# Performance work log

Measured on AMD Instinct MI355X. Metric: run time of the kernel, lower is better.

## Reference

```python
import jax, jax.numpy as jnp
import numpy as np

T, B = 128, 256
WD, TD, RD, M = 300, 64, 64, 512
G = 5 * M  # 5 gates: i, f_down, f_left, o, u


def setup_inputs() -> dict:
    key = jax.random.key(0)
    ks = jax.random.split(key, 13)
    s = 0.05  # weight scale for numerical sanity
    return {
        "word": jax.random.normal(ks[0], (T, B, WD), jnp.float32),
        "tag": jax.random.normal(ks[1], (T, B, TD), jnp.float32),
        "rel": jax.random.normal(ks[2], (T, B, RD), jnp.float32),
        "k": jax.random.normal(ks[3], (T, B, M), jnp.float32),
        "q": jax.random.normal(ks[4], (T, B, M), jnp.float32),
        "h0": jnp.zeros((B, M), jnp.float32),
        "c0": jnp.zeros((B, M), jnp.float32),
        "Ww": jax.random.normal(ks[5], (WD, G), jnp.float32) * s,
        "Wt": jax.random.normal(ks[6], (TD, G), jnp.float32) * s,
        "Wr": jax.random.normal(ks[7], (RD, G), jnp.float32) * s,
        "Wk": jax.random.normal(ks[8], (M, G), jnp.float32) * s,
        "Wh": jax.random.normal(ks[9], (M, G), jnp.float32) * s,
        "b": jax.random.normal(ks[10], (G,), jnp.float32) * s,
    }


def reference(word, tag, rel, k, q, h0, c0, Ww, Wt, Wr, Wk, Wh, b):
    mem = h0.shape[-1]
    # Fuse all non-recurrent projections for all 5 gates into one pass:
    # [T,B,5M] preactivations from word/tag/rel/k (the per-child inputs).
    xp = (jnp.einsum('tbd,dg->tbg', word, Ww)
          + jnp.einsum('tbd,dg->tbg', tag, Wt)
          + jnp.einsum('tbd,dg->tbg', rel, Wr)
          + jnp.einsum('tbd,dg->tbg', k, Wk)
          + b)

    def step(carry, inp):
        h, c = carry
        xpt, qt = inp  # [B,5M], [B,M]
        g = xpt + h @ Wh
        gi, gfd, gfl, go, gu = (g[..., 0*mem:1*mem], g[..., 1*mem:2*mem],
                                g[..., 2*mem:3*mem], g[..., 3*mem:4*mem],
                                g[..., 4*mem:5*mem])
        i_ = jax.nn.sigmoid(gi)
        f_down = jax.nn.sigmoid(gfd)
        f_left = jax.nn.sigmoid(gfl)
        o_ = jax.nn.sigmoid(go)
        u_ = jnp.tanh(gu)
        c_new = i_ * u_ + f_down * qt + f_left * c
        h_new = o_ * jnp.tanh(c_new)
        return (h_new, c_new), None

    (h, c), _ = jax.lax.scan(step, (h0, c0), (xp, q))
    # node_forward returns (k, q) = (h, c) after consuming all children
    return jnp.concatenate([h, c], axis=-1)  # [B, 2*M]
```

## Files before the change

kernel.cpp:

```cpp
#include <hip/hip_runtime.h>
#include <hip/hip_bf16.h>

#define TT   128
#define BB   256
#define MM   512
#define GG   2560
#define K1P  960

typedef __attribute__((ext_vector_type(8))) short bf16x8;
typedef __attribute__((ext_vector_type(4))) short bf16x4;
typedef __attribute__((ext_vector_type(4))) float f32x4;

__device__ __forceinline__ float bf2f(unsigned short u){
  union { unsigned u; float f; } v; v.u = ((unsigned)u) << 16; return v.f;
}
__device__ __forceinline__ unsigned short f2bf(float f){
  union { float f; unsigned u; } v; v.f = f;
  unsigned r = v.u + 0x7fffu + ((v.u >> 16) & 1u);
  return (unsigned short)(r >> 16);
}
__device__ __forceinline__ float sigmoidf_(float x){ return 1.f/(1.f + __expf(-x)); }
__device__ __forceinline__ float tanhf_(float x){
  x = fminf(15.f, fmaxf(-15.f, x));
  float e = __expf(2.f*x);
  return (e - 1.f)/(e + 1.f);
}

__device__ __forceinline__ void store_coh4(void* p, unsigned v){
  asm volatile("global_store_dword %0, %1, off sc0 sc1" :: "v"(p), "v"(v) : "memory");
}
__device__ __forceinline__ unsigned load_coh_u32(const unsigned* p){
  unsigned r;
  asm volatile("global_load_dword %0, %1, off sc0 sc1" : "=v"(r) : "v"(p) : "memory");
  asm volatile("s_waitcnt vmcnt(0)" ::: "memory");
  return r;
}
__device__ __forceinline__ bf16x8 load_h16(const void* p){
  bf16x8 r;
  asm volatile("global_load_dwordx4 %0, %1, off sc0 sc1" : "=v"(r) : "v"(p) : "memory");
  return r;
}
__device__ __forceinline__ void store_h32(void* p, unsigned v){
  asm volatile("global_store_dword %0, %1, off sc0 sc1" :: "v"(p), "v"(v) : "memory");
}

__device__ __forceinline__ void gll16(const unsigned short* g, unsigned short* l){
  __builtin_amdgcn_global_load_lds(
      (const __attribute__((address_space(1))) void*)(g),
      (__attribute__((address_space(3))) void*)(l),
      16, 0, 0);
}


__global__ __launch_bounds__(256) void stage_a(const float* __restrict__ word,
                                               const float* __restrict__ tag,
                                               const float* __restrict__ rel,
                                               const float* __restrict__ kin,
                                               unsigned short* __restrict__ A){
  long id = (long)blockIdx.x * 256 + threadIdx.x;
  int row = (int)(id / 120);
  int c8  = (int)(id % 120) * 8;
  bf16x8 o;
  #pragma unroll
  for (int j = 0; j < 8; ++j){
    int col = c8 + j; float v;
    if      (col < 300) v = word[(long)row*300 + col];
    else if (col < 364) v = tag [(long)row*64  + col-300];
    else if (col < 428) v = rel [(long)row*64  + col-364];
    else if (col < 940) v = kin [(long)row*512 + col-428];
    else v = 0.f;
    o[j] = (short)f2bf(v);
  }
  *reinterpret_cast<bf16x8*>(A + (long)row*K1P + c8) = o;
}

__global__ __launch_bounds__(256) void stage_wt(const float* __restrict__ Ww,
                                                const float* __restrict__ Wt,
                                                const float* __restrict__ Wr,
                                                const float* __restrict__ Wk,
                                                unsigned short* __restrict__ WT){
  long id = (long)blockIdx.x * 256 + threadIdx.x;
  int kk = (int)(id % K1P);
  int n  = (int)(id / K1P);
  float v;
  if      (kk < 300) v = Ww[(long)kk*GG + n];
  else if (kk < 364) v = Wt[(long)(kk-300)*GG + n];
  else if (kk < 428) v = Wr[(long)(kk-364)*GG + n];
  else if (kk < 940) v = Wk[(long)(kk-428)*GG + n];
  else v = 0.f;
  WT[(long)n*K1P + kk] = f2bf(v);
}

__global__ __launch_bounds__(256) void stage_wht(const float* __restrict__ Wh,
                                                 unsigned short* __restrict__ WhT){
  long id = (long)blockIdx.x * 256 + threadIdx.x;
  int kk = (int)(id % MM);
  int n  = (int)(id / MM);
  WhT[(long)n*MM + kk] = f2bf(Wh[(long)kk*GG + n]);
}

__global__ __launch_bounds__(256) void init_h(const float* __restrict__ h0,
                                              unsigned short* __restrict__ hb){
  int id = blockIdx.x * 256 + threadIdx.x;
  hb[id] = f2bf(h0[id]);
}

__global__ __launch_bounds__(256) void gemm_xp(const unsigned short* __restrict__ A,
                                               const unsigned short* __restrict__ WT,
                                               const float* __restrict__ bias,
                                               unsigned short* __restrict__ XP){
  __shared__ unsigned short As[128*64];
  __shared__ unsigned short Bs[128*64];
  const int tid  = threadIdx.x;
  const int wave = tid >> 6, lane = tid & 63;
  const int wr   = wave >> 1, wc = wave & 1;
  const int lrow = lane & 15, lhi = lane >> 4;

  const int swz = (blockIdx.x & 7) * (5120 / 8) + (blockIdx.x >> 3);
  const long row0 = (long)(swz & 255) * 128;
  const long col0 = (long)(swz >> 8) * 128;

  const int srow = wave*8 + (lane >> 3);
  const int scol = (((lane & 7) ^ (lane >> 3)) * 8);
  const unsigned short* gaB = A  + (row0 + srow)*K1P + scol;
  const unsigned short* gbB = WT + (col0 + srow)*K1P + scol;

  f32x4 acc[4][4] = {};
  for (int ks = 0; ks < 15; ++ks){
    const int k0 = ks * 64;
    __syncthreads();
    #pragma unroll
    for (int s = 0; s < 4; ++s){
      gll16(gaB + (long)s*32*K1P + k0, As + (s*32 + wave*8)*64);
      gll16(gbB + (long)s*32*K1P + k0, Bs + (s*32 + wave*8)*64);
    }
    __syncthreads();
    bf16x8 af[2][4], bfr[2][4];
    const int sx = (lrow & 7) * 8;
    #pragma unroll
    for (int kk = 0; kk < 2; ++kk){
      #pragma unroll
      for (int mi = 0; mi < 4; ++mi)
        af[kk][mi] = *reinterpret_cast<const bf16x8*>(
            As + (wr*64 + mi*16 + lrow)*64 + ((kk*32 + lhi*8) ^ sx));
      #pragma unroll
      for (int ni = 0; ni < 4; ++ni)
        bfr[kk][ni] = *reinterpret_cast<const bf16x8*>(
            Bs + (wc*64 + ni*16 + lrow)*64 + ((kk*32 + lhi*8) ^ sx));
    }
    #pragma unroll
    for (int kk = 0; kk < 2; ++kk)
      #pragma unroll
      for (int mi = 0; mi < 4; ++mi)
        #pragma unroll
        for (int ni = 0; ni < 4; ++ni)
          acc[mi][ni] = __builtin_amdgcn_mfma_f32_16x16x32_bf16(af[kk][mi], bfr[kk][ni], acc[mi][ni], 0, 0, 0);
  }
  const int t     = (int)(row0 >> 8);
  const int brow0 = (int)(row0 & 255);
  #pragma unroll
  for (int ni = 0; ni < 4; ++ni){
    const int col = (int)col0 + wc*64 + ni*16 + lrow;
    const float bv = bias[col];
    #pragma unroll
    for (int mi = 0; mi < 4; ++mi){
      const int b4 = brow0 + wr*64 + mi*16 + lhi*4;
      bf16x4 pk;
      #pragma unroll
      for (int j = 0; j < 4; ++j) pk[j] = (short)f2bf(acc[mi][ni][j] + bv);
      *reinterpret_cast<bf16x4*>(XP + ((long)t*GG + col)*BB + b4) = pk;
    }
  }
}

__global__ __launch_bounds__(256, 1) void lstm_fused(const unsigned short* __restrict__ XP,
                                                     const float* __restrict__ q,
                                                     const unsigned short* __restrict__ WhT,
                                                     const float* __restrict__ c0,
                                                     unsigned short* __restrict__ hb0,
                                                     unsigned short* __restrict__ hb1,
                                                     float* __restrict__ out,
                                                     unsigned* __restrict__ cnts){
  __shared__ float Part[4][5][2][16][20];
  const int tid  = threadIdx.x;
  const int w    = tid >> 6, lane = tid & 63;
  const int lrow = lane & 15, lhi = lane >> 4;
  const int bt = blockIdx.x >> 5, mc = blockIdx.x & 31;
  const int b0 = bt * 32, m0 = mc * 16;
  unsigned* cnt = cnts + bt * 64;

  bf16x8 Breg[5][4];
  #pragma unroll
  for (int g = 0; g < 5; ++g)
    #pragma unroll
    for (int kf = 0; kf < 4; ++kf)
      Breg[g][kf] = *reinterpret_cast<const bf16x8*>(
          WhT + (long)(g*MM + m0 + lrow)*MM + w*128 + kf*32 + lhi*8);

  const int bl = tid >> 3, mi2 = (tid & 7) * 2;
  const int rt2 = bl >> 4, brow = bl & 15;
  const int gb = b0 + bl, gm = m0 + mi2;
  float cx = c0[(long)gb*MM + gm];
  float cy = c0[(long)gb*MM + gm + 1];

  long oj[5];
  #pragma unroll
  for (int j = 0; j < 5; ++j) oj[j] = ((long)j*MM + gm)*BB + gb;
  const long qb0 = (long)gb*MM + gm;
  const long XSTEP = (long)GG*BB, QSTEP = (long)BB*MM;

  unsigned short xv[5][2]; float qx, qy;
  #pragma unroll
  for (int j = 0; j < 5; ++j){
    xv[j][0] = XP[oj[j]];
    xv[j][1] = XP[oj[j] + BB];
  }
  qx = q[qb0];
  qy = q[qb0 + 1];
  long xo = XSTEP, qo = QSTEP;

  for (int t = 0; t < TT; ++t){
    const unsigned short* hc = (t & 1) ? hb1 : hb0;
    unsigned short*       hn = (t & 1) ? hb0 : hb1;

    bf16x8 af[2][4];
    #pragma unroll
    for (int kf = 0; kf < 4; ++kf)
      #pragma unroll
      for (int rt = 0; rt < 2; ++rt)
        af[rt][kf] = load_h16(hc + (long)(b0 + rt*16 + lrow)*MM + w*128 + kf*32 + lhi*8);

    f32x4 acc[5][2] = {};
    #pragma unroll
    for (int kf = 0; kf < 4; ++kf){
      __builtin_amdgcn_sched_barrier(0);
      if      (kf == 0) asm volatile("s_waitcnt vmcnt(6)" ::: "memory");
      else if (kf == 1) asm volatile("s_waitcnt vmcnt(4)" ::: "memory");
      else if (kf == 2) asm volatile("s_waitcnt vmcnt(2)" ::: "memory");
      else              asm volatile("s_waitcnt vmcnt(0)" ::: "memory");
      __builtin_amdgcn_sched_barrier(0);
      #pragma unroll
      for (int rt = 0; rt < 2; ++rt)
        #pragma unroll
        for (int g = 0; g < 5; ++g)
          acc[g][rt] = __builtin_amdgcn_mfma_f32_16x16x32_bf16(af[rt][kf], Breg[g][kf], acc[g][rt], 0, 0, 0);
    }

    #pragma unroll
    for (int g = 0; g < 5; ++g)
      #pragma unroll
      for (int rt = 0; rt < 2; ++rt)
        *reinterpret_cast<f32x4*>(&Part[w][g][rt][lrow][lhi*4]) = acc[g][rt];
    __syncthreads();

    float gv[5][2];
    #pragma unroll
    for (int g = 0; g < 5; ++g)
      #pragma unroll
      for (int x = 0; x < 2; ++x)
        gv[g][x] = Part[0][g][rt2][mi2+x][brow] + Part[1][g][rt2][mi2+x][brow]
                 + Part[2][g][rt2][mi2+x][brow] + Part[3][g][rt2][mi2+x][brow]
                 + bf2f(xv[g][x]);

    float hx, hy;
    {
      const float i_ = sigmoidf_(gv[0][0]);
      const float fd = sigmoidf_(gv[1][0]);
      const float fl = sigmoidf_(gv[2][0]);
      const float o_ = sigmoidf_(gv[3][0]);
      const float u_ = tanhf_(gv[4][0]);
      const float cn = i_*u_ + fd*qx + fl*cx;
      cx = cn; hx = o_*tanhf_(cn);
    }
    {
      const float i_ = sigmoidf_(gv[0][1]);
      const float fd = sigmoidf_(gv[1][1]);
      const float fl = sigmoidf_(gv[2][1]);
      const float o_ = sigmoidf_(gv[3][1]);
      const float u_ = tanhf_(gv[4][1]);
      const float cn = i_*u_ + fd*qy + fl*cy;
      cy = cn; hy = o_*tanhf_(cn);
    }

    const unsigned hv = (unsigned)f2bf(hx) | ((unsigned)f2bf(hy) << 16);
    if (t < TT - 1){
      store_h32(hn + (long)gb*MM + gm, hv);
    } else {
      out[(long)gb*1024 + gm]           = hx;
      out[(long)gb*1024 + gm + 1]       = hy;
      out[(long)gb*1024 + 512 + gm]     = cx;
      out[(long)gb*1024 + 512 + gm + 1] = cy;
    }

    if (t < TT - 1){
      #pragma unroll
      for (int j = 0; j < 5; ++j){
        xv[j][0] = XP[xo + oj[j]];
        xv[j][1] = XP[xo + oj[j] + BB];
      }
      qx = q[qo + qb0];
      qy = q[qo + qb0 + 1];
      xo += XSTEP; qo += QSTEP;
    }

    if (t != TT - 1){
      __syncthreads();
      if (tid == 0){
        __hip_atomic_fetch_add(cnt, 1u, __ATOMIC_RELAXED, __HIP_MEMORY_SCOPE_AGENT);
        const unsigned target = (unsigned)(t + 1) * 32u;
        unsigned spins = 0;
        while (load_coh_u32(cnt) < target){
          __builtin_amdgcn_s_sleep(1);
          if (++spins > (1u << 20)) break;
        }
      }
      __syncthreads();
    }
  }
}

extern "C" void kernel_launch(void* const* d_in, const int* in_sizes, int n_in,
                              void* d_out, int out_size, void* d_ws, size_t ws_size,
                              hipStream_t stream){
  (void)in_sizes; (void)n_in; (void)out_size; (void)ws_size;
  const float* word = (const float*)d_in[0];
  const float* tag  = (const float*)d_in[1];
  const float* rel  = (const float*)d_in[2];
  const float* kin  = (const float*)d_in[3];
  const float* q    = (const float*)d_in[4];
  const float* h0   = (const float*)d_in[5];
  const float* c0   = (const float*)d_in[6];
  const float* Ww   = (const float*)d_in[7];
  const float* Wt   = (const float*)d_in[8];
  const float* Wr   = (const float*)d_in[9];
  const float* Wk   = (const float*)d_in[10];
  const float* Wh   = (const float*)d_in[11];
  const float* bias = (const float*)d_in[12];
  float* out = (float*)d_out;

  char* ws = (char*)d_ws;
  size_t off = 0;
  auto alloc = [&](size_t bytes)->void*{
    void* p = ws + off; off = (off + bytes + 255) & ~(size_t)255; return p;
  };
  unsigned short* Abf = (unsigned short*)alloc((size_t)TT*BB*K1P*2);
  unsigned short* WT  = (unsigned short*)alloc((size_t)GG*K1P*2);
  unsigned short* WhT = (unsigned short*)alloc((size_t)GG*MM*2);
  unsigned short* XP  = (unsigned short*)alloc((size_t)TT*BB*GG*2);
  unsigned short* hb0 = (unsigned short*)alloc((size_t)BB*MM*2);
  unsigned short* hb1 = (unsigned short*)alloc((size_t)BB*MM*2);
  unsigned*       cnt = (unsigned*)alloc(8 * 64 * sizeof(unsigned));

  hipMemsetAsync(cnt, 0, 8 * 64 * sizeof(unsigned), stream);

  stage_a  <<<dim3((TT*BB*(K1P/8) + 255)/256), 256, 0, stream>>>(word, tag, rel, kin, Abf);
  stage_wt <<<dim3((GG*K1P + 255)/256),        256, 0, stream>>>(Ww, Wt, Wr, Wk, WT);
  stage_wht<<<dim3((GG*MM + 255)/256),         256, 0, stream>>>(Wh, WhT);
  init_h   <<<dim3((BB*MM + 255)/256),         256, 0, stream>>>(h0, hb0);

  gemm_xp<<<dim3(5120), 256, 0, stream>>>(Abf, WT, bias, XP);

  lstm_fused<<<dim3(256), 256, 0, stream>>>(XP, q, WhT, c0, hb0, hb1, out, cnt);
}
```

Before: 773.1 us.

## Fuse input projection GEMM into recurrent LSTM kernel, drop XP buffer

Removes the separate gemm_xp kernel and its large bf16 XP intermediate. Each block of the persistent recurrent kernel now keeps its slice of the input-projection weights in registers and computes the input projection for its timestep with MFMAs inside the time loop, before the recurrent h@Wh product. K is padded to 1024 so the weight slice divides evenly across waves. This cuts the global write and read of XP but adds projection work and A-row loads to the serial per-timestep critical path, and increases register pressure.

```diff
diff --git a/kernel.cpp b/kernel.cpp
--- a/kernel.cpp
+++ b/kernel.cpp
@@ -5,7 +5,7 @@
 #define BB   256
 #define MM   512
 #define GG   2560
-#define K1P  960
+#define K1P  1024
 
 typedef __attribute__((ext_vector_type(8))) short bf16x8;
 typedef __attribute__((ext_vector_type(4))) short bf16x4;
@@ -26,9 +26,6 @@
   return (e - 1.f)/(e + 1.f);
 }
 
-__device__ __forceinline__ void store_coh4(void* p, unsigned v){
-  asm volatile("global_store_dword %0, %1, off sc0 sc1" :: "v"(p), "v"(v) : "memory");
-}
 __device__ __forceinline__ unsigned load_coh_u32(const unsigned* p){
   unsigned r;
   asm volatile("global_load_dword %0, %1, off sc0 sc1" : "=v"(r) : "v"(p) : "memory");
@@ -43,12 +40,10 @@
 __device__ __forceinline__ void store_h32(void* p, unsigned v){
   asm volatile("global_store_dword %0, %1, off sc0 sc1" :: "v"(p), "v"(v) : "memory");
 }
-
-__device__ __forceinline__ void gll16(const unsigned short* g, unsigned short* l){
-  __builtin_amdgcn_global_load_lds(
-      (const __attribute__((address_space(1))) void*)(g),
-      (__attribute__((address_space(3))) void*)(l),
-      16, 0, 0);
+__device__ __forceinline__ bf16x8 ldg16(const void* p){
+  bf16x8 r;
+  asm volatile("global_load_dwordx4 %0, %1, off" : "=v"(r) : "v"(p) : "memory");
+  return r;
 }
 
 
@@ -58,8 +53,8 @@
                                                const float* __restrict__ kin,
                                                unsigned short* __restrict__ A){
   long id = (long)blockIdx.x * 256 + threadIdx.x;
-  int row = (int)(id / 120);
-  int c8  = (int)(id % 120) * 8;
+  int row = (int)(id >> 7);
+  int c8  = (int)(id & 127) * 8;
   bf16x8 o;
   #pragma unroll
   for (int j = 0; j < 8; ++j){
@@ -80,8 +75,8 @@
                                                 const float* __restrict__ Wk,
                                                 unsigned short* __restrict__ WT){
   long id = (long)blockIdx.x * 256 + threadIdx.x;
-  int kk = (int)(id % K1P);
-  int n  = (int)(id / K1P);
+  int kk = (int)(id & 1023);
+  int n  = (int)(id >> 10);
   float v;
   if      (kk < 300) v = Ww[(long)kk*GG + n];
   else if (kk < 364) v = Wt[(long)(kk-300)*GG + n];
@@ -105,77 +100,11 @@
   hb[id] = f2bf(h0[id]);
 }
 
-__global__ __launch_bounds__(256) void gemm_xp(const unsigned short* __restrict__ A,
-                                               const unsigned short* __restrict__ WT,
-                                               const float* __restrict__ bias,
-                                               unsigned short* __restrict__ XP){
-  __shared__ unsigned short As[128*64];
-  __shared__ unsigned short Bs[128*64];
-  const int tid  = threadIdx.x;
-  const int wave = tid >> 6, lane = tid & 63;
-  const int wr   = wave >> 1, wc = wave & 1;
-  const int lrow = lane & 15, lhi = lane >> 4;
-
-  const int swz = (blockIdx.x & 7) * (5120 / 8) + (blockIdx.x >> 3);
-  const long row0 = (long)(swz & 255) * 128;
-  const long col0 = (long)(swz >> 8) * 128;
-
-  const int srow = wave*8 + (lane >> 3);
-  const int scol = (((lane & 7) ^ (lane >> 3)) * 8);
-  const unsigned short* gaB = A  + (row0 + srow)*K1P + scol;
-  const unsigned short* gbB = WT + (col0 + srow)*K1P + scol;
-
-  f32x4 acc[4][4] = {};
-  for (int ks = 0; ks < 15; ++ks){
-    const int k0 = ks * 64;
-    __syncthreads();
-    #pragma unroll
-    for (int s = 0; s < 4; ++s){
-      gll16(gaB + (long)s*32*K1P + k0, As + (s*32 + wave*8)*64);
-      gll16(gbB + (long)s*32*K1P + k0, Bs + (s*32 + wave*8)*64);
-    }
-    __syncthreads();
-    bf16x8 af[2][4], bfr[2][4];
-    const int sx = (lrow & 7) * 8;
-    #pragma unroll
-    for (int kk = 0; kk < 2; ++kk){
-      #pragma unroll
-      for (int mi = 0; mi < 4; ++mi)
-        af[kk][mi] = *reinterpret_cast<const bf16x8*>(
-            As + (wr*64 + mi*16 + lrow)*64 + ((kk*32 + lhi*8) ^ sx));
-      #pragma unroll
-      for (int ni = 0; ni < 4; ++ni)
-        bfr[kk][ni] = *reinterpret_cast<const bf16x8*>(
-            Bs + (wc*64 + ni*16 + lrow)*64 + ((kk*32 + lhi*8) ^ sx));
-    }
-    #pragma unroll
-    for (int kk = 0; kk < 2; ++kk)
-      #pragma unroll
-      for (int mi = 0; mi < 4; ++mi)
-        #pragma unroll
-        for (int ni = 0; ni < 4; ++ni)
-          acc[mi][ni] = __builtin_amdgcn_mfma_f32_16x16x32_bf16(af[kk][mi], bfr[kk][ni], acc[mi][ni], 0, 0, 0);
-  }
-  const int t     = (int)(row0 >> 8);
-  const int brow0 = (int)(row0 & 255);
-  #pragma unroll
-  for (int ni = 0; ni < 4; ++ni){
-    const int col = (int)col0 + wc*64 + ni*16 + lrow;
-    const float bv = bias[col];
-    #pragma unroll
-    for (int mi = 0; mi < 4; ++mi){
-      const int b4 = brow0 + wr*64 + mi*16 + lhi*4;
-      bf16x4 pk;
-      #pragma unroll
-      for (int j = 0; j < 4; ++j) pk[j] = (short)f2bf(acc[mi][ni][j] + bv);
-      *reinterpret_cast<bf16x4*>(XP + ((long)t*GG + col)*BB + b4) = pk;
-    }
-  }
-}
-
-__global__ __launch_bounds__(256, 1) void lstm_fused(const unsigned short* __restrict__ XP,
+__global__ __launch_bounds__(256, 1) void lstm_fused(const unsigned short* __restrict__ Abf,
                                                      const float* __restrict__ q,
+                                                     const unsigned short* __restrict__ WT,
                                                      const unsigned short* __restrict__ WhT,
+                                                     const float* __restrict__ bias,
                                                      const float* __restrict__ c0,
                                                      unsigned short* __restrict__ hb0,
                                                      unsigned short* __restrict__ hb1,
@@ -189,12 +118,19 @@
   const int b0 = bt * 32, m0 = mc * 16;
   unsigned* cnt = cnts + bt * 64;
 
-  bf16x8 Breg[5][4];
+  bf16x8 Wreg[5][8];
   #pragma unroll
   for (int g = 0; g < 5; ++g)
     #pragma unroll
+    for (int c = 0; c < 8; ++c)
+      Wreg[g][c] = *reinterpret_cast<const bf16x8*>(
+          WT + (long)(g*MM + m0 + lrow)*K1P + w*256 + c*32 + lhi*8);
+  bf16x8 Hreg[5][4];
+  #pragma unroll
+  for (int g = 0; g < 5; ++g)
+    #pragma unroll
     for (int kf = 0; kf < 4; ++kf)
-      Breg[g][kf] = *reinterpret_cast<const bf16x8*>(
+      Hreg[g][kf] = *reinterpret_cast<const bf16x8*>(
           WhT + (long)(g*MM + m0 + lrow)*MM + w*128 + kf*32 + lhi*8);
 
   const int bl = tid >> 3, mi2 = (tid & 7) * 2;
@@ -203,26 +139,31 @@
   float cx = c0[(long)gb*MM + gm];
   float cy = c0[(long)gb*MM + gm + 1];
 
-  long oj[5];
+  float bq[5][2];
   #pragma unroll
-  for (int j = 0; j < 5; ++j) oj[j] = ((long)j*MM + gm)*BB + gb;
+  for (int g = 0; g < 5; ++g){
+    bq[g][0] = bias[g*MM + gm];
+    bq[g][1] = bias[g*MM + gm + 1];
+  }
+
+  const unsigned short* aB0 = Abf + (long)(b0 + 0*16 + lrow)*K1P + w*256 + lhi*8;
+  const unsigned short* aB1 = Abf + (long)(b0 + 1*16 + lrow)*K1P + w*256 + lhi*8;
+  const long ASTEP = (long)BB * K1P;
   const long qb0 = (long)gb*MM + gm;
-  const long XSTEP = (long)GG*BB, QSTEP = (long)BB*MM;
-
-  unsigned short xv[5][2]; float qx, qy;
-  #pragma unroll
-  for (int j = 0; j < 5; ++j){
-    xv[j][0] = XP[oj[j]];
-    xv[j][1] = XP[oj[j] + BB];
-  }
-  qx = q[qb0];
-  qy = q[qb0 + 1];
-  long xo = XSTEP, qo = QSTEP;
+  const long QSTEP = (long)BB*MM;
+  float qx = q[qb0], qy = q[qb0 + 1];
+  long qo = QSTEP;
 
   for (int t = 0; t < TT; ++t){
     const unsigned short* hc = (t & 1) ? hb1 : hb0;
     unsigned short*       hn = (t & 1) ? hb0 : hb1;
 
+    bf16x8 aw[2][8];
+    #pragma unroll
+    for (int c = 0; c < 8; ++c){
+      aw[0][c] = ldg16(aB0 + c*32);
+      aw[1][c] = ldg16(aB1 + c*32);
+    }
     bf16x8 af[2][4];
     #pragma unroll
     for (int kf = 0; kf < 4; ++kf)
@@ -231,6 +172,17 @@
         af[rt][kf] = load_h16(hc + (long)(b0 + rt*16 + lrow)*MM + w*128 + kf*32 + lhi*8);
 
     f32x4 acc[5][2] = {};
+    __builtin_amdgcn_sched_barrier(0);
+    asm volatile("s_waitcnt vmcnt(8)" ::: "memory");
+    __builtin_amdgcn_sched_barrier(0);
+    #pragma unroll
+    for (int c = 0; c < 8; ++c)
+      #pragma unroll
+      for (int rt = 0; rt < 2; ++rt)
+        #pragma unroll
+        for (int g = 0; g < 5; ++g)
+          acc[g][rt] = __builtin_amdgcn_mfma_f32_16x16x32_bf16(aw[rt][c], Wreg[g][c], acc[g][rt], 0, 0, 0);
+
     #pragma unroll
     for (int kf = 0; kf < 4; ++kf){
       __builtin_amdgcn_sched_barrier(0);
@@ -243,7 +195,7 @@
       for (int rt = 0; rt < 2; ++rt)
         #pragma unroll
         for (int g = 0; g < 5; ++g)
-          acc[g][rt] = __builtin_amdgcn_mfma_f32_16x16x32_bf16(af[rt][kf], Breg[g][kf], acc[g][rt], 0, 0, 0);
+          acc[g][rt] = __builtin_amdgcn_mfma_f32_16x16x32_bf16(af[rt][kf], Hreg[g][kf], acc[g][rt], 0, 0, 0);
     }
 
     #pragma unroll
@@ -260,7 +212,7 @@
       for (int x = 0; x < 2; ++x)
         gv[g][x] = Part[0][g][rt2][mi2+x][brow] + Part[1][g][rt2][mi2+x][brow]
                  + Part[2][g][rt2][mi2+x][brow] + Part[3][g][rt2][mi2+x][brow]
-                 + bf2f(xv[g][x]);
+                 + bq[g][x];
 
     float hx, hy;
     {
@@ -293,14 +245,10 @@
     }
 
     if (t < TT - 1){
-      #pragma unroll
-      for (int j = 0; j < 5; ++j){
-        xv[j][0] = XP[xo + oj[j]];
-        xv[j][1] = XP[xo + oj[j] + BB];
-      }
       qx = q[qo + qb0];
       qy = q[qo + qb0 + 1];
-      xo += XSTEP; qo += QSTEP;
+      qo += QSTEP;
+      aB0 += ASTEP; aB1 += ASTEP;
     }
 
     if (t != TT - 1){
@@ -346,19 +294,16 @@
   unsigned short* Abf = (unsigned short*)alloc((size_t)TT*BB*K1P*2);
   unsigned short* WT  = (unsigned short*)alloc((size_t)GG*K1P*2);
   unsigned short* WhT = (unsigned short*)alloc((size_t)GG*MM*2);
-  unsigned short* XP  = (unsigned short*)alloc((size_t)TT*BB*GG*2);
   unsigned short* hb0 = (unsigned short*)alloc((size_t)BB*MM*2);
   unsigned short* hb1 = (unsigned short*)alloc((size_t)BB*MM*2);
   unsigned*       cnt = (unsigned*)alloc(8 * 64 * sizeof(unsigned));
 
   hipMemsetAsync(cnt, 0, 8 * 64 * sizeof(unsigned), stream);
 
-  stage_a  <<<dim3((TT*BB*(K1P/8) + 255)/256), 256, 0, stream>>>(word, tag, rel, kin, Abf);
-  stage_wt <<<dim3((GG*K1P + 255)/256),        256, 0, stream>>>(Ww, Wt, Wr, Wk, WT);
-  stage_wht<<<dim3((GG*MM + 255)/256),         256, 0, stream>>>(Wh, WhT);
-  init_h   <<<dim3((BB*MM + 255)/256),         256, 0, stream>>>(h0, hb0);
-
-  gemm_xp<<<dim3(5120), 256, 0, stream>>>(Abf, WT, bias, XP);
-
-  lstm_fused<<<dim3(256), 256, 0, stream>>>(XP, q, WhT, c0, hb0, hb1, out, cnt);
-}
+  stage_a  <<<dim3((int)(((long)TT*BB*(K1P/8) + 255)/256)), 256, 0, stream>>>(word, tag, rel, kin, Abf);
+  stage_wt <<<dim3((int)(((long)GG*K1P + 255)/256)),        256, 0, stream>>>(Ww, Wt, Wr, Wk, WT);
+  stage_wht<<<dim3((GG*MM + 255)/256),                      256, 0, stream>>>(Wh, WhT);
+  init_h   <<<dim3((BB*MM + 255)/256),                      256, 0, stream>>>(h0, hb0);
+
+  lstm_fused<<<dim3(256), 256, 0, stream>>>(Abf, q, WT, WhT, bias, c0, hb0, hb1, out, cnt);
+}
```

Result: faster. 756.5 us (-2.2%).
